# Kernel tuning notes

Hardware: AMD Instinct MI355X
Metric: run time of the kernel (lower is better)

Reference implementation:

```python
import jax, jax.numpy as jnp
import numpy as np

N_NODES = 100000
N_EDGES = 1600000
IN_C, HID_C, OUT_C = 64, 64, 32


def setup_inputs() -> dict:
    key = jax.random.key(0)
    ks = jax.random.split(key, 6)
    x = jax.random.normal(ks[0], (N_NODES, IN_C), dtype=jnp.float32)
    edge_index = jax.random.randint(ks[1], (2, N_EDGES), 0, N_NODES, dtype=jnp.int64)
    edge_weight = jax.random.uniform(ks[2], (N_EDGES,), dtype=jnp.float32)
    # Glorot-ish init for the two GCNConv weight matrices, zero bias (PyG default)
    W1 = jax.random.normal(ks[3], (IN_C, HID_C), dtype=jnp.float32) / np.sqrt(IN_C)
    b1 = jnp.zeros((HID_C,), dtype=jnp.float32)
    W2 = jax.random.normal(ks[4], (HID_C, OUT_C), dtype=jnp.float32) / np.sqrt(HID_C)
    b2 = jnp.zeros((OUT_C,), dtype=jnp.float32)
    return {"x": x, "edge_index": edge_index, "edge_weight": edge_weight,
            "W1": W1, "b1": b1, "W2": W2, "b2": b2}


def _gcn_conv(x, src, dst, w, W, b):
    """PyG GCNConv: add self-loops (weight 1), symmetric D^-1/2 (A+I) D^-1/2 norm,
    then aggregate transformed features into destination nodes, plus bias."""
    n = x.shape[0]
    loop = jnp.arange(n, dtype=src.dtype)
    s = jnp.concatenate([src, loop])
    d = jnp.concatenate([dst, loop])
    wl = jnp.concatenate([w, jnp.ones((n,), dtype=x.dtype)])
    deg = jax.ops.segment_sum(wl, d, num_segments=n)            # [N]
    dinv = jnp.where(deg > 0, jax.lax.rsqrt(deg), 0.0)
    norm = dinv[s] * wl * dinv[d]                               # [E+N]
    xw = x @ W                                                  # [N, C_out]
    msg = norm[:, None] * xw[s]                                 # gather + scale
    return jax.ops.segment_sum(msg, d, num_segments=n) + b      # scatter-add


def reference(x, edge_index, edge_weight, W1, b1, W2, b2):
    src, dst = edge_index[0], edge_index[1]
    h = _gcn_conv(x, src, dst, edge_weight, W1, b1)
    h = jax.nn.relu(h)
    # dropout(p=0.5, training=self.training): identity in eval mode
    return _gcn_conv(h, src, dst, edge_weight, W2, b2)
```

## Files before the change

kernel.cpp:

```cpp
#include <hip/hip_runtime.h>

#define N_NODES 100000
#define N_EDGES 1600000
#define IN_C 64
#define HID_C 64
#define OUT_C 32

#define NB 391
#define BSHIFT 8
#define BMASK 255
#define SEG_CAP 4864
#define EPB 4096
#define BIN_BLOCKS ((N_EDGES + EPB - 1) / EPB)
#define G1_BLOCKS ((N_NODES + 63) / 64)
#define SMASK 0x1FFFF
#define FIXSCALE 34359738368.0f

__device__ __forceinline__ unsigned int bpack(float a, float b) {
    unsigned int ua = __float_as_uint(a);
    ua += 0x7FFFu + ((ua >> 16) & 1u);
    unsigned int ub = __float_as_uint(b);
    ub += 0x7FFFu + ((ub >> 16) & 1u);
    return (ua >> 16) | (ub & 0xFFFF0000u);
}
__device__ __forceinline__ float2 bup(unsigned int v) {
    return make_float2(__uint_as_float(v << 16), __uint_as_float(v & 0xFFFF0000u));
}


struct BinSh {
    int meta[EPB];
    int hist[NB];
    int gbase[NB];
};
struct G1Sh {
    float XsT[64][64];
    float Ws[64][64];
};
union FusedSh { BinSh b; G1Sh g; };

__global__ void __launch_bounds__(256) fused1_kernel(
    const int* __restrict__ src, const int* __restrict__ dst,
    const float* __restrict__ w, int* __restrict__ gcnt, int2* __restrict__ seg,
    const float* __restrict__ X, const float* __restrict__ W,
    unsigned int* __restrict__ XWu) {
    __shared__ FusedSh sh;
    int tid = threadIdx.x;
    if (blockIdx.x < BIN_BLOCKS) {
        for (int i = tid; i < NB; i += 256) sh.b.hist[i] = 0;
        __syncthreads();
        int e0 = blockIdx.x * EPB;
        int n = min(EPB, N_EDGES - e0);
        const int4* dst4 = (const int4*)(dst + e0);
        int n4 = n >> 2;
        for (int i = tid; i < n4; i += 256) {
            int4 d = dst4[i];
            int b0 = d.x >> BSHIFT, b1 = d.y >> BSHIFT;
            int b2 = d.z >> BSHIFT, b3 = d.w >> BSHIFT;
            sh.b.meta[0 * n4 + i] = atomicAdd(&sh.b.hist[b0], 1);
            sh.b.meta[1 * n4 + i] = atomicAdd(&sh.b.hist[b1], 1);
            sh.b.meta[2 * n4 + i] = atomicAdd(&sh.b.hist[b2], 1);
            sh.b.meta[3 * n4 + i] = atomicAdd(&sh.b.hist[b3], 1);
        }
        __syncthreads();
        for (int b = tid; b < NB; b += 256) {
            int c = sh.b.hist[b];
            sh.b.gbase[b] = c ? atomicAdd(&gcnt[b], c) : 0;
        }
        __syncthreads();
        const int4* src4 = (const int4*)(src + e0);
        const float4* w4 = (const float4*)(w + e0);
        for (int i = tid; i < n4; i += 256) {
            int4 s = src4[i];
            int4 d = dst4[i];
            float4 ww = w4[i];
#define FL_ONE(K, SS, DD, WW)                                              \
            {                                                              \
                int b = (DD) >> BSHIFT;                                    \
                int pos = sh.b.gbase[b] + sh.b.meta[K * n4 + i];           \
                if (pos < SEG_CAP)                                         \
                    seg[(size_t)b * SEG_CAP + pos] =                       \
                        make_int2((SS) | (((DD) & BMASK) << 17),           \
                                  __float_as_int(WW));                     \
            }
            FL_ONE(0, s.x, d.x, ww.x)
            FL_ONE(1, s.y, d.y, ww.y)
            FL_ONE(2, s.z, d.z, ww.z)
            FL_ONE(3, s.w, d.w, ww.w)
#undef FL_ONE
        }
    } else {
        {
            const float4* Wv = (const float4*)W;
            float4* Wsv = (float4*)&sh.g.Ws[0][0];
            for (int i = tid; i < 1024; i += 256) Wsv[i] = Wv[i];
        }
        int row0 = (blockIdx.x - BIN_BLOCKS) * 64;
        int rmax = N_NODES - row0;
        for (int i = tid; i < 64 * 16; i += 256) {
            int r = i & 63, kq = i >> 6;
            float4 v = (r < rmax) ? ((const float4*)(X + (size_t)(row0 + r) * IN_C))[kq]
                                  : make_float4(0.f, 0.f, 0.f, 0.f);
            sh.g.XsT[4 * kq + 0][r] = v.x;
            sh.g.XsT[4 * kq + 1][r] = v.y;
            sh.g.XsT[4 * kq + 2][r] = v.z;
            sh.g.XsT[4 * kq + 3][r] = v.w;
        }
        __syncthreads();
        int tr = tid >> 4, tc = tid & 15;
        float acc[4][4] = {};
        float a[4], bb[4];
#pragma unroll 8
        for (int k = 0; k < 64; ++k) {
            *(float4*)a = *(const float4*)&sh.g.XsT[k][4 * tr];
            *(float4*)bb = *(const float4*)&sh.g.Ws[k][4 * tc];
#pragma unroll
            for (int i = 0; i < 4; ++i)
#pragma unroll
                for (int j = 0; j < 4; ++j) acc[i][j] += a[i] * bb[j];
        }
#pragma unroll
        for (int i = 0; i < 4; ++i) {
            int rl = 4 * tr + i;
            if (rl < rmax) {
                int row = row0 + rl;
                uint2 o;
                o.x = bpack(acc[i][0], acc[i][1]);
                o.y = bpack(acc[i][2], acc[i][3]);
                ((uint2*)XWu)[(size_t)row * 16 + tc] = o;
            }
        }
    }
}


__global__ void __launch_bounds__(1024) bsort_kernel(const int* __restrict__ gcnt,
                                                     const int2* __restrict__ seg,
                                                     int2* __restrict__ seg2,
                                                     float* __restrict__ dinv,
                                                     int2* __restrict__ rowRC,
                                                     unsigned int* __restrict__ XWs) {
    __shared__ unsigned long long packed[256];
    __shared__ int meta[SEG_CAP];
    __shared__ int sarr[256];
    __shared__ int ofs0[256];
    __shared__ float dinvsh[256];
    int tid = threadIdx.x, b = blockIdx.x;
    int n = min(gcnt[b], SEG_CAP);
    const int2* sp = seg + (size_t)b * SEG_CAP;
    if (tid < 256) packed[tid] = 0ULL;
    __syncthreads();
    for (int i = tid; i < n; i += 1024) {
        int2 r = sp[i];
        int dl = (r.x >> 17) & BMASK;
        unsigned long long fixw =
            (unsigned long long)(__int_as_float(r.y) * FIXSCALE);
        unsigned long long old = atomicAdd(&packed[dl], (1ULL << 48) | fixw);
        meta[i] = dl | ((int)(old >> 48) << 8);
    }
    __syncthreads();
    int myc = 0, padc = 0;
    if (tid < 256) {
        unsigned long long p = packed[tid];
        myc = (int)(p >> 48);
        float degw = (float)((double)(p & ((1ULL << 48) - 1)) * (1.0 / (double)FIXSCALE));
        float dv = rsqrtf(1.0f + degw);
        dinvsh[tid] = dv;
        int node = (b << BSHIFT) + tid;
        if (node < N_NODES) dinv[node] = dv;
        padc = (myc + 1) & ~1;
        sarr[tid] = padc;
    }
    __syncthreads();
    for (int off = 1; off < 256; off <<= 1) {
        int tmp = 0;
        if (tid < 256 && tid >= off) tmp = sarr[tid - off];
        __syncthreads();
        if (tid < 256) sarr[tid] += tmp;
        __syncthreads();
    }
    if (tid < 256) {
        int excl = sarr[tid] - padc;
        int node = (b << BSHIFT) + tid;
        if (node < N_NODES) rowRC[node] = make_int2(b * SEG_CAP + excl, myc);
        ofs0[tid] = excl;
    }
    __syncthreads();
    int2* op = seg2 + (size_t)b * SEG_CAP;
    for (int i = tid; i < n; i += 1024) {
        int2 r = sp[i];
        int m = meta[i];
        int dl = m & BMASK, rank = m >> 8;
        op[ofs0[dl] + rank] = r;
    }
    int baseRow = b << BSHIFT;
    int rowsHere = min(256, N_NODES - baseRow);
    uint4* XW4 = (uint4*)XWs;
    for (int i = tid; i < rowsHere * 8; i += 1024) {
        int nl = i >> 3;
        float s = dinvsh[nl];
        uint4 v = XW4[(size_t)(baseRow + nl) * 8 + (i & 7)];
        float2 f;
        f = bup(v.x); v.x = bpack(f.x * s, f.y * s);
        f = bup(v.y); v.y = bpack(f.x * s, f.y * s);
        f = bup(v.z); v.z = bpack(f.x * s, f.y * s);
        f = bup(v.w); v.w = bpack(f.x * s, f.y * s);
        XW4[(size_t)(baseRow + nl) * 8 + (i & 7)] = v;
    }
}


__global__ void __launch_bounds__(256) agg1_kernel(const int2* __restrict__ rowRC,
                                                   const int2* __restrict__ seg2,
                                                   const unsigned int* __restrict__ XWs,
                                                   const float* __restrict__ dinv,
                                                   const float* __restrict__ b1,
                                                   const float* __restrict__ W2,
                                                   unsigned int* __restrict__ HWs) {
    __shared__ float Hs[16][68];
    __shared__ float Ws2[64][32];
    int tid = threadIdx.x;
    {
        const float4* Wv = (const float4*)W2;
        float4* Wsv = (float4*)&Ws2[0][0];
        for (int i = tid; i < 512; i += 256) Wsv[i] = Wv[i];
    }
    int l16 = tid & 15;
    int nl = tid >> 4;
    int d = blockIdx.x * 16 + nl;
    const uint2* XW2 = (const uint2*)XWs;
    float did = dinv[d];
    float4 bv = ((const float4*)b1)[l16];
    uint2 sv = XW2[(size_t)d * 16 + l16];
    float2 f0 = bup(sv.x), f1 = bup(sv.y);
    float a0 = bv.x + did * f0.x, a1 = bv.y + did * f0.y;
    float a2 = bv.z + did * f1.x, a3 = bv.w + did * f1.y;
    int2 rc = rowRC[d];
    int nc = rc.y;
    const int2* sp = seg2 + rc.x;
    const int4* sp4 = (const int4*)sp;
    int e = 0;
    for (; e + 8 <= nc; e += 8) {
        int4 q0 = sp4[(e >> 1) + 0], q1 = sp4[(e >> 1) + 1];
        int4 q2 = sp4[(e >> 1) + 2], q3 = sp4[(e >> 1) + 3];
        int s0 = q0.x & SMASK, s1 = q0.z & SMASK, s2 = q1.x & SMASK, s3 = q1.z & SMASK;
        int s4 = q2.x & SMASK, s5 = q2.z & SMASK, s6 = q3.x & SMASK, s7 = q3.z & SMASK;
        uint2 r0 = XW2[(size_t)s0 * 16 + l16];
        uint2 r1 = XW2[(size_t)s1 * 16 + l16];
        uint2 r2 = XW2[(size_t)s2 * 16 + l16];
        uint2 r3 = XW2[(size_t)s3 * 16 + l16];
        uint2 r4 = XW2[(size_t)s4 * 16 + l16];
        uint2 r5 = XW2[(size_t)s5 * 16 + l16];
        uint2 r6 = XW2[(size_t)s6 * 16 + l16];
        uint2 r7 = XW2[(size_t)s7 * 16 + l16];
        float c0 = __int_as_float(q0.y) * did, c1 = __int_as_float(q0.w) * did;
        float c2 = __int_as_float(q1.y) * did, c3 = __int_as_float(q1.w) * did;
        float c4 = __int_as_float(q2.y) * did, c5 = __int_as_float(q2.w) * did;
        float c6 = __int_as_float(q3.y) * did, c7 = __int_as_float(q3.w) * did;
        float2 v;
#define ACC1(R, C)                                                         \
        v = bup(R.x); a0 += (C) * v.x; a1 += (C) * v.y;                    \
        v = bup(R.y); a2 += (C) * v.x; a3 += (C) * v.y;
        ACC1(r0, c0) ACC1(r1, c1) ACC1(r2, c2) ACC1(r3, c3)
        ACC1(r4, c4) ACC1(r5, c5) ACC1(r6, c6) ACC1(r7, c7)
    }
    for (; e + 2 <= nc; e += 2) {
        int4 q = sp4[e >> 1];
        int s0 = q.x & SMASK, s1 = q.z & SMASK;
        uint2 r0 = XW2[(size_t)s0 * 16 + l16];
        uint2 r1 = XW2[(size_t)s1 * 16 + l16];
        float c0 = __int_as_float(q.y) * did, c1 = __int_as_float(q.w) * did;
        float2 v;
        ACC1(r0, c0) ACC1(r1, c1)
    }
    if (e < nc) {
        int2 p = sp[e];
        int s = p.x & SMASK;
        float c = __int_as_float(p.y) * did;
        uint2 r = XW2[(size_t)s * 16 + l16];
        float2 v;
        ACC1(r, c)
    }
#undef ACC1
    *(float4*)&Hs[nl][4 * l16] = make_float4(fmaxf(a0, 0.f), fmaxf(a1, 0.f),
                                             fmaxf(a2, 0.f), fmaxf(a3, 0.f));
    __syncthreads();
    int c0i = l16 * 2;
    float o0 = 0.f, o1 = 0.f;
#pragma unroll
    for (int k = 0; k < 64; ++k) {
        float hk = Hs[nl][k];
        float2 wv = *(const float2*)&Ws2[k][c0i];
        o0 += hk * wv.x;
        o1 += hk * wv.y;
    }
    ((unsigned int*)HWs)[(size_t)d * 16 + l16] = bpack(o0 * did, o1 * did);
}


__global__ void __launch_bounds__(256) agg2_kernel(const int2* __restrict__ rowRC,
                                                   const int2* __restrict__ seg2,
                                                   const unsigned int* __restrict__ HWs,
                                                   const float* __restrict__ dinv,
                                                   const float* __restrict__ b2,
                                                   float* __restrict__ out) {
    int l8 = threadIdx.x & 7;
    int d = blockIdx.x * 32 + (threadIdx.x >> 3);
    if (d >= N_NODES) return;
    const uint2* HW2 = (const uint2*)HWs;
    float did = dinv[d];
    float4 bv = ((const float4*)b2)[l8];
    uint2 sv = HW2[(size_t)d * 8 + l8];
    float2 f0 = bup(sv.x), f1 = bup(sv.y);
    float a0 = bv.x + did * f0.x, a1 = bv.y + did * f0.y;
    float a2 = bv.z + did * f1.x, a3 = bv.w + did * f1.y;
    int2 rc = rowRC[d];
    int nc = rc.y;
    const int2* sp = seg2 + rc.x;
    const int4* sp4 = (const int4*)sp;
    int e = 0;
    for (; e + 8 <= nc; e += 8) {
        int4 q0 = sp4[(e >> 1) + 0], q1 = sp4[(e >> 1) + 1];
        int4 q2 = sp4[(e >> 1) + 2], q3 = sp4[(e >> 1) + 3];
        int s0 = q0.x & SMASK, s1 = q0.z & SMASK, s2 = q1.x & SMASK, s3 = q1.z & SMASK;
        int s4 = q2.x & SMASK, s5 = q2.z & SMASK, s6 = q3.x & SMASK, s7 = q3.z & SMASK;
        uint2 r0 = HW2[(size_t)s0 * 8 + l8];
        uint2 r1 = HW2[(size_t)s1 * 8 + l8];
        uint2 r2 = HW2[(size_t)s2 * 8 + l8];
        uint2 r3 = HW2[(size_t)s3 * 8 + l8];
        uint2 r4 = HW2[(size_t)s4 * 8 + l8];
        uint2 r5 = HW2[(size_t)s5 * 8 + l8];
        uint2 r6 = HW2[(size_t)s6 * 8 + l8];
        uint2 r7 = HW2[(size_t)s7 * 8 + l8];
        float c0 = __int_as_float(q0.y) * did, c1 = __int_as_float(q0.w) * did;
        float c2 = __int_as_float(q1.y) * did, c3 = __int_as_float(q1.w) * did;
        float c4 = __int_as_float(q2.y) * did, c5 = __int_as_float(q2.w) * did;
        float c6 = __int_as_float(q3.y) * did, c7 = __int_as_float(q3.w) * did;
        float2 v;
#define ACC2(R, C)                                                         \
        v = bup(R.x); a0 += (C) * v.x; a1 += (C) * v.y;                    \
        v = bup(R.y); a2 += (C) * v.x; a3 += (C) * v.y;
        ACC2(r0, c0) ACC2(r1, c1) ACC2(r2, c2) ACC2(r3, c3)
        ACC2(r4, c4) ACC2(r5, c5) ACC2(r6, c6) ACC2(r7, c7)
    }
    for (; e + 2 <= nc; e += 2) {
        int4 q = sp4[e >> 1];
        int s0 = q.x & SMASK, s1 = q.z & SMASK;
        uint2 r0 = HW2[(size_t)s0 * 8 + l8];
        uint2 r1 = HW2[(size_t)s1 * 8 + l8];
        float c0 = __int_as_float(q.y) * did, c1 = __int_as_float(q.w) * did;
        float2 v;
        ACC2(r0, c0) ACC2(r1, c1)
    }
    if (e < nc) {
        int2 p = sp[e];
        int s = p.x & SMASK;
        float c = __int_as_float(p.y) * did;
        uint2 r = HW2[(size_t)s * 8 + l8];
        float2 v;
        ACC2(r, c)
    }
#undef ACC2
    ((float4*)out)[(size_t)d * 8 + l8] = make_float4(a0, a1, a2, a3);
}


extern "C" void kernel_launch(void* const* d_in, const int* in_sizes, int n_in,
                              void* d_out, int out_size, void* d_ws, size_t ws_size,
                              hipStream_t stream) {
    const float* x = (const float*)d_in[0];
    const int* edge_index = (const int*)d_in[1];
    const float* ew = (const float*)d_in[2];
    const float* W1 = (const float*)d_in[3];
    const float* b1 = (const float*)d_in[4];
    const float* W2 = (const float*)d_in[5];
    const float* b2 = (const float*)d_in[6];
    float* out = (float*)d_out;

    const int* src = edge_index;
    const int* dst = edge_index + N_EDGES;

    char* ws = (char*)d_ws;
    size_t off = 0;
    auto carve = [&](size_t bytes) -> void* {
        void* p = ws + off;
        off += (bytes + 255) & ~(size_t)255;
        return p;
    };

    int* gcnt = (int*)carve(NB * 4);
    float* dinv = (float*)carve((size_t)N_NODES * 4);
    int2* rowRC = (int2*)carve((size_t)N_NODES * 8);
    int2* seg = (int2*)carve((size_t)NB * SEG_CAP * 8);
    int2* seg2 = (int2*)carve((size_t)NB * SEG_CAP * 8);
    unsigned int* XWs = (unsigned int*)carve((size_t)N_NODES * 32 * 4);
    unsigned int* HWs = (unsigned int*)carve((size_t)N_NODES * 16 * 4);

    hipMemsetAsync(gcnt, 0, NB * 4, stream);
    fused1_kernel<<<BIN_BLOCKS + G1_BLOCKS, 256, 0, stream>>>(src, dst, ew, gcnt, seg,
                                                              x, W1, XWs);
    bsort_kernel<<<NB, 1024, 0, stream>>>(gcnt, seg, seg2, dinv, rowRC, XWs);
    agg1_kernel<<<N_NODES / 16, 256, 0, stream>>>(rowRC, seg2, XWs, dinv, b1, W2, HWs);
    agg2_kernel<<<(N_NODES + 31) / 32, 256, 0, stream>>>(rowRC, seg2, HWs, dinv, b2, out);
}
```

Baseline: 207.2 us.

## Move degree sum to global atomics and fuse X@W1 GEMM into sort kernel

Weighted degrees are now accumulated with global float atomics during edge binning, replacing the fixed-point 64-bit packed shared atomics in the sort. With degrees ready earlier, the X@W1 GEMM moves into the sort kernel's extra blocks and applies the dinv scale directly. This drops the separate read-modify-write pass over XW that bsort used to do. Binning uses smaller chunks per block, and the GEMM runs four 64-row tiles per 1024-thread block. The cost is 1.6M global float atomics into a 100K-entry degree array, whose summation order is nondeterministic.

Result: slower. 294.9 us (+42.3%).

```diff
diff --git a/kernel.cpp b/kernel.cpp
--- a/kernel.cpp
+++ b/kernel.cpp
@@ -10,11 +10,10 @@
 #define BSHIFT 8
 #define BMASK 255
 #define SEG_CAP 4864
-#define EPB 4096
+#define EPB 2048
 #define BIN_BLOCKS ((N_EDGES + EPB - 1) / EPB)
-#define G1_BLOCKS ((N_NODES + 63) / 64)
+#define G2_BLOCKS ((N_NODES + 255) / 256)
 #define SMASK 0x1FFFF
-#define FIXSCALE 34359738368.0f
 
 __device__ __forceinline__ unsigned int bpack(float a, float b) {
     unsigned int ua = __float_as_uint(a);
@@ -28,91 +27,143 @@
 }
 
 
-struct BinSh {
-    int meta[EPB];
-    int hist[NB];
-    int gbase[NB];
-};
-struct G1Sh {
-    float XsT[64][64];
-    float Ws[64][64];
-};
-union FusedSh { BinSh b; G1Sh g; };
-
-__global__ void __launch_bounds__(256) fused1_kernel(
+__global__ void __launch_bounds__(256) bin_kernel(
     const int* __restrict__ src, const int* __restrict__ dst,
     const float* __restrict__ w, int* __restrict__ gcnt, int2* __restrict__ seg,
-    const float* __restrict__ X, const float* __restrict__ W,
-    unsigned int* __restrict__ XWu) {
-    __shared__ FusedSh sh;
+    float* __restrict__ degw) {
+    __shared__ int meta[EPB];
+    __shared__ int hist[NB];
+    __shared__ int gbase[NB];
     int tid = threadIdx.x;
-    if (blockIdx.x < BIN_BLOCKS) {
-        for (int i = tid; i < NB; i += 256) sh.b.hist[i] = 0;
-        __syncthreads();
-        int e0 = blockIdx.x * EPB;
-        int n = min(EPB, N_EDGES - e0);
-        const int4* dst4 = (const int4*)(dst + e0);
-        int n4 = n >> 2;
-        for (int i = tid; i < n4; i += 256) {
-            int4 d = dst4[i];
-            int b0 = d.x >> BSHIFT, b1 = d.y >> BSHIFT;
-            int b2 = d.z >> BSHIFT, b3 = d.w >> BSHIFT;
-            sh.b.meta[0 * n4 + i] = atomicAdd(&sh.b.hist[b0], 1);
-            sh.b.meta[1 * n4 + i] = atomicAdd(&sh.b.hist[b1], 1);
-            sh.b.meta[2 * n4 + i] = atomicAdd(&sh.b.hist[b2], 1);
-            sh.b.meta[3 * n4 + i] = atomicAdd(&sh.b.hist[b3], 1);
-        }
-        __syncthreads();
-        for (int b = tid; b < NB; b += 256) {
-            int c = sh.b.hist[b];
-            sh.b.gbase[b] = c ? atomicAdd(&gcnt[b], c) : 0;
-        }
-        __syncthreads();
-        const int4* src4 = (const int4*)(src + e0);
-        const float4* w4 = (const float4*)(w + e0);
-        for (int i = tid; i < n4; i += 256) {
-            int4 s = src4[i];
-            int4 d = dst4[i];
-            float4 ww = w4[i];
+    for (int i = tid; i < NB; i += 256) hist[i] = 0;
+    __syncthreads();
+    int e0 = blockIdx.x * EPB;
+    int n = min(EPB, N_EDGES - e0);
+    const int4* dst4 = (const int4*)(dst + e0);
+    int n4 = n >> 2;
+    for (int i = tid; i < n4; i += 256) {
+        int4 d = dst4[i];
+        meta[0 * n4 + i] = atomicAdd(&hist[d.x >> BSHIFT], 1);
+        meta[1 * n4 + i] = atomicAdd(&hist[d.y >> BSHIFT], 1);
+        meta[2 * n4 + i] = atomicAdd(&hist[d.z >> BSHIFT], 1);
+        meta[3 * n4 + i] = atomicAdd(&hist[d.w >> BSHIFT], 1);
+    }
+    __syncthreads();
+    for (int b = tid; b < NB; b += 256) {
+        int c = hist[b];
+        gbase[b] = c ? atomicAdd(&gcnt[b], c) : 0;
+    }
+    __syncthreads();
+    const int4* src4 = (const int4*)(src + e0);
+    const float4* w4 = (const float4*)(w + e0);
+    for (int i = tid; i < n4; i += 256) {
+        int4 s = src4[i];
+        int4 d = dst4[i];
+        float4 ww = w4[i];
 #define FL_ONE(K, SS, DD, WW)                                              \
-            {                                                              \
-                int b = (DD) >> BSHIFT;                                    \
-                int pos = sh.b.gbase[b] + sh.b.meta[K * n4 + i];           \
-                if (pos < SEG_CAP)                                         \
-                    seg[(size_t)b * SEG_CAP + pos] =                       \
-                        make_int2((SS) | (((DD) & BMASK) << 17),           \
-                                  __float_as_int(WW));                     \
-            }
-            FL_ONE(0, s.x, d.x, ww.x)
-            FL_ONE(1, s.y, d.y, ww.y)
-            FL_ONE(2, s.z, d.z, ww.z)
-            FL_ONE(3, s.w, d.w, ww.w)
+        {                                                                  \
+            int b = (DD) >> BSHIFT;                                        \
+            int pos = gbase[b] + meta[K * n4 + i];                         \
+            atomicAdd(&degw[DD], (WW));                                    \
+            if (pos < SEG_CAP)                                             \
+                seg[(size_t)b * SEG_CAP + pos] =                           \
+                    make_int2((SS) | (((DD) & BMASK) << 17),               \
+                              __float_as_int(WW));                         \
+        }
+        FL_ONE(0, s.x, d.x, ww.x)
+        FL_ONE(1, s.y, d.y, ww.y)
+        FL_ONE(2, s.z, d.z, ww.z)
+        FL_ONE(3, s.w, d.w, ww.w)
 #undef FL_ONE
+    }
+}
+
+
+struct SortSh {
+    int cnt[256];
+    int meta2[SEG_CAP];
+    int sarr[256];
+    int ofs0[256];
+};
+struct GemmSh {
+    float Ws[64][64];
+    float XsT[4][64][64];
+};
+union K2Sh { SortSh s; GemmSh g; };
+
+__global__ void __launch_bounds__(1024) sortgemm_kernel(
+    const int* __restrict__ gcnt, const int2* __restrict__ seg,
+    int2* __restrict__ seg2, int2* __restrict__ rowRC,
+    const float* __restrict__ X, const float* __restrict__ W1,
+    const float* __restrict__ degw, float* __restrict__ dinv,
+    unsigned int* __restrict__ XWs) {
+    __shared__ K2Sh sh;
+    int tid = threadIdx.x;
+    if (blockIdx.x < NB) {
+        int b = blockIdx.x;
+        int n = min(gcnt[b], SEG_CAP);
+        const int2* sp = seg + (size_t)b * SEG_CAP;
+        if (tid < 256) sh.s.cnt[tid] = 0;
+        __syncthreads();
+        for (int i = tid; i < n; i += 1024) {
+            int2 r = sp[i];
+            int dl = (r.x >> 17) & BMASK;
+            sh.s.meta2[i] = dl | (atomicAdd(&sh.s.cnt[dl], 1) << 8);
+        }
+        __syncthreads();
+        int myc = 0, padc = 0;
+        if (tid < 256) {
+            myc = sh.s.cnt[tid];
+            padc = (myc + 1) & ~1;
+            sh.s.sarr[tid] = padc;
+        }
+        __syncthreads();
+        for (int off = 1; off < 256; off <<= 1) {
+            int tmp = 0;
+            if (tid < 256 && tid >= off) tmp = sh.s.sarr[tid - off];
+            __syncthreads();
+            if (tid < 256) sh.s.sarr[tid] += tmp;
+            __syncthreads();
+        }
+        if (tid < 256) {
+            int excl = sh.s.sarr[tid] - padc;
+            int node = (b << BSHIFT) + tid;
+            if (node < N_NODES) rowRC[node] = make_int2(b * SEG_CAP + excl, myc);
+            sh.s.ofs0[tid] = excl;
+        }
+        __syncthreads();
+        int2* op = seg2 + (size_t)b * SEG_CAP;
+        for (int i = tid; i < n; i += 1024) {
+            int2 r = sp[i];
+            int m = sh.s.meta2[i];
+            op[sh.s.ofs0[m & BMASK] + (m >> 8)] = r;
         }
     } else {
         {
-            const float4* Wv = (const float4*)W;
-            float4* Wsv = (float4*)&sh.g.Ws[0][0];
-            for (int i = tid; i < 1024; i += 256) Wsv[i] = Wv[i];
-        }
-        int row0 = (blockIdx.x - BIN_BLOCKS) * 64;
+            const float4* Wv = (const float4*)W1;
+            ((float4*)&sh.g.Ws[0][0])[tid] = Wv[tid];
+        }
+        int sub = tid >> 8;
+        int t = tid & 255;
+        int row0 = (blockIdx.x - NB) * 256 + sub * 64;
         int rmax = N_NODES - row0;
-        for (int i = tid; i < 64 * 16; i += 256) {
+        float (*XsT)[64] = sh.g.XsT[sub];
+        for (int i = t; i < 64 * 16; i += 256) {
             int r = i & 63, kq = i >> 6;
             float4 v = (r < rmax) ? ((const float4*)(X + (size_t)(row0 + r) * IN_C))[kq]
                                   : make_float4(0.f, 0.f, 0.f, 0.f);
-            sh.g.XsT[4 * kq + 0][r] = v.x;
-            sh.g.XsT[4 * kq + 1][r] = v.y;
-            sh.g.XsT[4 * kq + 2][r] = v.z;
-            sh.g.XsT[4 * kq + 3][r] = v.w;
-        }
-        __syncthreads();
-        int tr = tid >> 4, tc = tid & 15;
+            XsT[4 * kq + 0][r] = v.x;
+            XsT[4 * kq + 1][r] = v.y;
+            XsT[4 * kq + 2][r] = v.z;
+            XsT[4 * kq + 3][r] = v.w;
+        }
+        __syncthreads();
+        int tr = t >> 4, tc = t & 15;
         float acc[4][4] = {};
         float a[4], bb[4];
 #pragma unroll 8
         for (int k = 0; k < 64; ++k) {
-            *(float4*)a = *(const float4*)&sh.g.XsT[k][4 * tr];
+            *(float4*)a = *(const float4*)&XsT[k][4 * tr];
             *(float4*)bb = *(const float4*)&sh.g.Ws[k][4 * tc];
 #pragma unroll
             for (int i = 0; i < 4; ++i)
@@ -124,88 +175,14 @@
             int rl = 4 * tr + i;
             if (rl < rmax) {
                 int row = row0 + rl;
+                float dv = rsqrtf(1.0f + degw[row]);
+                if (tc == 0) dinv[row] = dv;
                 uint2 o;
-                o.x = bpack(acc[i][0], acc[i][1]);
-                o.y = bpack(acc[i][2], acc[i][3]);
-                ((uint2*)XWu)[(size_t)row * 16 + tc] = o;
+                o.x = bpack(acc[i][0] * dv, acc[i][1] * dv);
+                o.y = bpack(acc[i][2] * dv, acc[i][3] * dv);
+                ((uint2*)XWs)[(size_t)row * 16 + tc] = o;
             }
         }
-    }
-}
-
-
-__global__ void __launch_bounds__(1024) bsort_kernel(const int* __restrict__ gcnt,
-                                                     const int2* __restrict__ seg,
-                                                     int2* __restrict__ seg2,
-                                                     float* __restrict__ dinv,
-                                                     int2* __restrict__ rowRC,
-                                                     unsigned int* __restrict__ XWs) {
-    __shared__ unsigned long long packed[256];
-    __shared__ int meta[SEG_CAP];
-    __shared__ int sarr[256];
-    __shared__ int ofs0[256];
-    __shared__ float dinvsh[256];
-    int tid = threadIdx.x, b = blockIdx.x;
-    int n = min(gcnt[b], SEG_CAP);
-    const int2* sp = seg + (size_t)b * SEG_CAP;
-    if (tid < 256) packed[tid] = 0ULL;
-    __syncthreads();
-    for (int i = tid; i < n; i += 1024) {
-        int2 r = sp[i];
-        int dl = (r.x >> 17) & BMASK;
-        unsigned long long fixw =
-            (unsigned long long)(__int_as_float(r.y) * FIXSCALE);
-        unsigned long long old = atomicAdd(&packed[dl], (1ULL << 48) | fixw);
-        meta[i] = dl | ((int)(old >> 48) << 8);
-    }
-    __syncthreads();
-    int myc = 0, padc = 0;
-    if (tid < 256) {
-        unsigned long long p = packed[tid];
-        myc = (int)(p >> 48);
-        float degw = (float)((double)(p & ((1ULL << 48) - 1)) * (1.0 / (double)FIXSCALE));
-        float dv = rsqrtf(1.0f + degw);
-        dinvsh[tid] = dv;
-        int node = (b << BSHIFT) + tid;
-        if (node < N_NODES) dinv[node] = dv;
-        padc = (myc + 1) & ~1;
-        sarr[tid] = padc;
-    }
-    __syncthreads();
-    for (int off = 1; off < 256; off <<= 1) {
-        int tmp = 0;
-        if (tid < 256 && tid >= off) tmp = sarr[tid - off];
-        __syncthreads();
-        if (tid < 256) sarr[tid] += tmp;
-        __syncthreads();
-    }
-    if (tid < 256) {
-        int excl = sarr[tid] - padc;
-        int node = (b << BSHIFT) + tid;
-        if (node < N_NODES) rowRC[node] = make_int2(b * SEG_CAP + excl, myc);
-        ofs0[tid] = excl;
-    }
-    __syncthreads();
-    int2* op = seg2 + (size_t)b * SEG_CAP;
-    for (int i = tid; i < n; i += 1024) {
-        int2 r = sp[i];
-        int m = meta[i];
-        int dl = m & BMASK, rank = m >> 8;
-        op[ofs0[dl] + rank] = r;
-    }
-    int baseRow = b << BSHIFT;
-    int rowsHere = min(256, N_NODES - baseRow);
-    uint4* XW4 = (uint4*)XWs;
-    for (int i = tid; i < rowsHere * 8; i += 1024) {
-        int nl = i >> 3;
-        float s = dinvsh[nl];
-        uint4 v = XW4[(size_t)(baseRow + nl) * 8 + (i & 7)];
-        float2 f;
-        f = bup(v.x); v.x = bpack(f.x * s, f.y * s);
-        f = bup(v.y); v.y = bpack(f.x * s, f.y * s);
-        f = bup(v.z); v.z = bpack(f.x * s, f.y * s);
-        f = bup(v.w); v.w = bpack(f.x * s, f.y * s);
-        XW4[(size_t)(baseRow + nl) * 8 + (i & 7)] = v;
     }
 }
 
@@ -389,6 +366,7 @@
     };
 
     int* gcnt = (int*)carve(NB * 4);
+    float* degw = (float*)carve((size_t)N_NODES * 4);
     float* dinv = (float*)carve((size_t)N_NODES * 4);
     int2* rowRC = (int2*)carve((size_t)N_NODES * 8);
     int2* seg = (int2*)carve((size_t)NB * SEG_CAP * 8);
@@ -396,10 +374,11 @@
     unsigned int* XWs = (unsigned int*)carve((size_t)N_NODES * 32 * 4);
     unsigned int* HWs = (unsigned int*)carve((size_t)N_NODES * 16 * 4);
 
-    hipMemsetAsync(gcnt, 0, NB * 4, stream);
-    fused1_kernel<<<BIN_BLOCKS + G1_BLOCKS, 256, 0, stream>>>(src, dst, ew, gcnt, seg,
-                                                              x, W1, XWs);
-    bsort_kernel<<<NB, 1024, 0, stream>>>(gcnt, seg, seg2, dinv, rowRC, XWs);
+    size_t zspan = (((size_t)NB * 4 + 255) & ~(size_t)255) + (size_t)N_NODES * 4;
+    hipMemsetAsync(gcnt, 0, zspan, stream);
+    bin_kernel<<<BIN_BLOCKS, 256, 0, stream>>>(src, dst, ew, gcnt, seg, degw);
+    sortgemm_kernel<<<NB + G2_BLOCKS, 1024, 0, stream>>>(gcnt, seg, seg2, rowRC,
+                                                         x, W1, degw, dinv, XWs);
     agg1_kernel<<<N_NODES / 16, 256, 0, stream>>>(rowRC, seg2, XWs, dinv, b1, W2, HWs);
     agg2_kernel<<<(N_NODES + 31) / 32, 256, 0, stream>>>(rowRC, seg2, HWs, dinv, b2, out);
 }
```

## Degree-sort nodes within each bucket to balance aggregation work; double edges per bin block

Applied to the files above, without the earlier changes.

The bucket-sort kernel now counting-sorts the 256 nodes of each bucket by in-degree and writes a per-bucket permutation. Both aggregation kernels take their destination node from this permutation, so the nodes sharing a wavefront have similar edge counts and spend fewer lanes idle on divergent loop trip counts. In exchange the sort kernel pays for an extra shared-memory scan and barriers, and the aggregation writes become scattered within each bucket. Separately, the edges handled per binning block go from 4096 to 8192, which halves the number of binning blocks.

Result: slower. 214.1 us (+3.3%).

```diff
diff --git a/kernel.cpp b/kernel.cpp
--- a/kernel.cpp
+++ b/kernel.cpp
@@ -10,7 +10,7 @@
 #define BSHIFT 8
 #define BMASK 255
 #define SEG_CAP 4864
-#define EPB 4096
+#define EPB 8192
 #define BIN_BLOCKS ((N_EDGES + EPB - 1) / EPB)
 #define G1_BLOCKS ((N_NODES + 63) / 64)
 #define SMASK 0x1FFFF
@@ -139,12 +139,14 @@
                                                      int2* __restrict__ seg2,
                                                      float* __restrict__ dinv,
                                                      int2* __restrict__ rowRC,
-                                                     unsigned int* __restrict__ XWs) {
+                                                     unsigned int* __restrict__ XWs,
+                                                     int* __restrict__ perm) {
     __shared__ unsigned long long packed[256];
     __shared__ int meta[SEG_CAP];
     __shared__ int sarr[256];
     __shared__ int ofs0[256];
     __shared__ float dinvsh[256];
+    __shared__ int dcnt[256];
     int tid = threadIdx.x, b = blockIdx.x;
     int n = min(gcnt[b], SEG_CAP);
     const int2* sp = seg + (size_t)b * SEG_CAP;
@@ -207,6 +209,30 @@
         f = bup(v.w); v.w = bpack(f.x * s, f.y * s);
         XW4[(size_t)(baseRow + nl) * 8 + (i & 7)] = v;
     }
+    __syncthreads();
+    if (tid < 256) dcnt[tid] = 0;
+    __syncthreads();
+    int key = 0, drank = 0;
+    int node = (b << BSHIFT) + tid;
+    bool valid = (tid < 256) && (node < N_NODES);
+    if (valid) {
+        key = min(myc, 255);
+        drank = atomicAdd(&dcnt[key], 1);
+    }
+    __syncthreads();
+    if (tid < 256) sarr[tid] = dcnt[tid];
+    __syncthreads();
+    for (int off = 1; off < 256; off <<= 1) {
+        int tmp = 0;
+        if (tid < 256 && tid >= off) tmp = sarr[tid - off];
+        __syncthreads();
+        if (tid < 256) sarr[tid] += tmp;
+        __syncthreads();
+    }
+    if (valid) {
+        int base = sarr[key] - dcnt[key];
+        perm[(b << BSHIFT) + base + drank] = node;
+    }
 }
 
 
@@ -216,6 +242,7 @@
                                                    const float* __restrict__ dinv,
                                                    const float* __restrict__ b1,
                                                    const float* __restrict__ W2,
+                                                   const int* __restrict__ perm,
                                                    unsigned int* __restrict__ HWs) {
     __shared__ float Hs[16][68];
     __shared__ float Ws2[64][32];
@@ -227,7 +254,7 @@
     }
     int l16 = tid & 15;
     int nl = tid >> 4;
-    int d = blockIdx.x * 16 + nl;
+    int d = perm[blockIdx.x * 16 + nl];
     const uint2* XW2 = (const uint2*)XWs;
     float did = dinv[d];
     float4 bv = ((const float4*)b1)[l16];
@@ -303,10 +330,10 @@
                                                    const unsigned int* __restrict__ HWs,
                                                    const float* __restrict__ dinv,
                                                    const float* __restrict__ b2,
+                                                   const int* __restrict__ perm,
                                                    float* __restrict__ out) {
     int l8 = threadIdx.x & 7;
-    int d = blockIdx.x * 32 + (threadIdx.x >> 3);
-    if (d >= N_NODES) return;
+    int d = perm[blockIdx.x * 32 + (threadIdx.x >> 3)];
     const uint2* HW2 = (const uint2*)HWs;
     float did = dinv[d];
     float4 bv = ((const float4*)b2)[l8];
@@ -391,6 +418,7 @@
     int* gcnt = (int*)carve(NB * 4);
     float* dinv = (float*)carve((size_t)N_NODES * 4);
     int2* rowRC = (int2*)carve((size_t)N_NODES * 8);
+    int* perm = (int*)carve((size_t)NB * 256 * 4);
     int2* seg = (int2*)carve((size_t)NB * SEG_CAP * 8);
     int2* seg2 = (int2*)carve((size_t)NB * SEG_CAP * 8);
     unsigned int* XWs = (unsigned int*)carve((size_t)N_NODES * 32 * 4);
@@ -399,7 +427,7 @@
     hipMemsetAsync(gcnt, 0, NB * 4, stream);
     fused1_kernel<<<BIN_BLOCKS + G1_BLOCKS, 256, 0, stream>>>(src, dst, ew, gcnt, seg,
                                                               x, W1, XWs);
-    bsort_kernel<<<NB, 1024, 0, stream>>>(gcnt, seg, seg2, dinv, rowRC, XWs);
-    agg1_kernel<<<N_NODES / 16, 256, 0, stream>>>(rowRC, seg2, XWs, dinv, b1, W2, HWs);
-    agg2_kernel<<<(N_NODES + 31) / 32, 256, 0, stream>>>(rowRC, seg2, HWs, dinv, b2, out);
-}
+    bsort_kernel<<<NB, 1024, 0, stream>>>(gcnt, seg, seg2, dinv, rowRC, XWs, perm);
+    agg1_kernel<<<N_NODES / 16, 256, 0, stream>>>(rowRC, seg2, XWs, dinv, b1, W2, perm, HWs);
+    agg2_kernel<<<(N_NODES + 31) / 32, 256, 0, stream>>>(rowRC, seg2, HWs, dinv, b2, perm, out);
+}
```
